# Performance work log

Hardware: AMD Instinct MI355X
Metric: run time of the kernel (lower is better)

## Reference

```python
import jax, jax.numpy as jnp
import numpy as np

R = 4            # num_runs
P_DROP = 0.2     # node dropout prob
BN_EPS = 1e-5
L = 2            # num_layers
D = 128          # hidden_channels
NA, NP_ = 50000, 100000
E = 500000


def setup_inputs() -> dict:
    key = jax.random.key(0)
    ks = jax.random.split(key, 20)
    s = 0.05
    x_author = jax.random.normal(ks[0], (NA, D), jnp.float32)
    x_paper = jax.random.normal(ks[1], (NP_, D), jnp.float32)
    # edge_index rows: [src, dst]
    ei_ap = jnp.stack([
        jax.random.randint(ks[2], (E,), 0, NA),
        jax.random.randint(ks[3], (E,), 0, NP_)]).astype(jnp.int64)
    ei_pa = jnp.stack([
        jax.random.randint(ks[4], (E,), 0, NP_),
        jax.random.randint(ks[5], (E,), 0, NA)]).astype(jnp.int64)
    # bernoulli(1-p) keep masks, one per run per node
    drop_author = (jax.random.uniform(ks[6], (R, NA)) < (1.0 - P_DROP)).astype(jnp.float32)
    drop_paper = (jax.random.uniform(ks[7], (R, NP_)) < (1.0 - P_DROP)).astype(jnp.float32)
    return {
        "x_author": x_author, "x_paper": x_paper,
        "ei_ap": ei_ap, "ei_pa": ei_pa,
        "drop_author": drop_author, "drop_paper": drop_paper,
        "lin_a_w": jax.random.normal(ks[8], (D, D)) * s,
        "lin_a_b": jnp.zeros((D,), jnp.float32),
        "lin_p_w": jax.random.normal(ks[9], (D, D)) * s,
        "lin_p_b": jnp.zeros((D,), jnp.float32),
        "W1": jax.random.normal(ks[10], (L, 2, D, D)) * s,
        "B1": jnp.zeros((L, 2, D), jnp.float32),
        "G": jnp.ones((L, 2, D), jnp.float32),
        "BT": jnp.zeros((L, 2, D), jnp.float32),
        "W2": jax.random.normal(ks[11], (L, 2, D, D)) * s,
        "B2": jnp.zeros((L, 2, D), jnp.float32),
        "EPS": jnp.zeros((L, 2), jnp.float32),  # GIN train_eps init 0
        "final_w": jax.random.normal(ks[12], (D, 4)) * s,
        "final_b": jnp.zeros((4,), jnp.float32),
    }


def _gin(x_src, x_dst, ei, eps, w1, b1, g, bt, w2, b2):
    # x_src: [Rs*Ns, D] flattened over runs; x_dst: [Rd*Nd, D]
    # scatter-sum neighbor messages into dst (only run-0 slots touched,
    # matching the original code which reuses the unexpanded edge_index)
    agg = jnp.zeros_like(x_dst).at[ei[1]].add(x_src[ei[0]])
    z = (1.0 + eps) * x_dst + agg
    h = z @ w1 + b1
    # BatchNorm1d, training-mode batch stats (biased variance)
    mu = h.mean(axis=0)
    var = ((h - mu) ** 2).mean(axis=0)
    h = (h - mu) * jax.lax.rsqrt(var + BN_EPS) * g + bt
    h = jax.nn.relu(h)
    return h @ w2 + b2


def reference(x_author, x_paper, ei_ap, ei_pa, drop_author, drop_paper,
              lin_a_w, lin_a_b, lin_p_w, lin_p_b,
              W1, B1, G, BT, W2, B2, EPS, final_w, final_b):
    inv_keep = 1.0 / (1.0 - P_DROP)
    # input projections, expand over runs, DropGNN node dropout
    h_a = x_author @ lin_a_w + lin_a_b                       # [Na, D]
    h_a = jnp.broadcast_to(h_a[None], (R,) + h_a.shape)      # [R, Na, D]
    h_a = h_a * drop_author[..., None] * inv_keep
    h_p = x_paper @ lin_p_w + lin_p_b
    h_p = jnp.broadcast_to(h_p[None], (R,) + h_p.shape)
    h_p = h_p * drop_paper[..., None] * inv_keep

    for l in range(L):
        xa = h_a.reshape(-1, D)
        xp = h_p.reshape(-1, D)
        # edge type 0: author -writes-> paper ; edge type 1: paper -> author
        new_p = _gin(xa, xp, ei_ap, EPS[l, 0], W1[l, 0], B1[l, 0], G[l, 0], BT[l, 0], W2[l, 0], B2[l, 0])
        new_a = _gin(xp, xa, ei_pa, EPS[l, 1], W1[l, 1], B1[l, 1], G[l, 1], BT[l, 1], W2[l, 1], B2[l, 1])
        h_a = jax.nn.relu(new_a.reshape(R, NA, D))
        h_p = jax.nn.relu(new_p.reshape(R, NP_, D))

    h = h_a.mean(axis=0)                                     # [Na, D]
    return h @ final_w + final_b                             # [Na, num_classes]
```

## Files before the change

### kernel.cpp

```cpp
#include <hip/hip_runtime.h>

#define NRUNS 4
#define NAU 50000
#define NPP 100000
#define NEDGE 500000
#define HD 128
#define INV_KEEP 1.25f
#define BN_EPS 1e-5f
#define LDA 136
#define NB_GEMM 1536

#define M_PROJ 0
#define M_GIN1 1
#define M_GIN2 2

typedef unsigned short bf16r;
typedef __attribute__((ext_vector_type(8))) short v8s;
typedef __attribute__((ext_vector_type(4))) float v4f;

__device__ inline float bf2f(bf16r u) {
    return __uint_as_float(((unsigned)u) << 16);
}
__device__ inline bf16r f2bf(float f) {
    __bf16 b = (__bf16)f;
    return __builtin_bit_cast(bf16r, b);
}

__global__ __launch_bounds__(256)
void zero_k(float* p, long n4) {
    long i = (long)blockIdx.x * 256 + threadIdx.x;
    long stride = (long)gridDim.x * 256;
    float4 z = make_float4(0.f, 0.f, 0.f, 0.f);
    for (; i < n4; i += stride) ((float4*)p)[i] = z;
}

__global__ __launch_bounds__(256)
void convw_k(const float* __restrict__ lin_a_w, const float* __restrict__ lin_p_w,
             const float* __restrict__ W1, const float* __restrict__ W2,
             bf16r* __restrict__ wt)
{
    int t = blockIdx.x >> 6;
    int e = (blockIdx.x & 63) * 256 + threadIdx.x;
    const float* src;
    if (t == 0) src = lin_a_w;
    else if (t == 1) src = lin_p_w;
    else if (t < 6) src = W1 + (size_t)(t - 2) * HD * HD;
    else src = W2 + (size_t)(t - 6) * HD * HD;
    int n = e >> 7, k = e & 127;
    wt[(size_t)t * HD * HD + e] = f2bf(src[(size_t)k * HD + n]);
}

__global__ __launch_bounds__(256)
void count_k(const int* __restrict__ ei, int E, int* cnt) {
    int e = blockIdx.x * 256 + threadIdx.x;
    if (e < E) atomicAdd(&cnt[ei[E + e]], 1);
}

__global__ __launch_bounds__(256)
void scan1_k(const int* __restrict__ in, int* out, int* partial, int n) {
    __shared__ int lds[256];
    int b = blockIdx.x, t = threadIdx.x;
    int base = b * 1024 + t * 4;
    int v0 = 0, v1 = 0, v2 = 0, v3 = 0;
    if (base + 3 < n) {
        int4 x = *(const int4*)(in + base);
        v0 = x.x; v1 = x.y; v2 = x.z; v3 = x.w;
    } else {
        if (base + 0 < n) v0 = in[base + 0];
        if (base + 1 < n) v1 = in[base + 1];
        if (base + 2 < n) v2 = in[base + 2];
        if (base + 3 < n) v3 = in[base + 3];
    }
    int s = v0 + v1 + v2 + v3;
    lds[t] = s;
    __syncthreads();
    for (int d = 1; d < 256; d <<= 1) {
        int x = (t >= d) ? lds[t - d] : 0;
        __syncthreads();
        lds[t] += x;
        __syncthreads();
    }
    int excl = lds[t] - s;
    if (base + 0 < n) out[base + 0] = excl;
    if (base + 1 < n) out[base + 1] = excl + v0;
    if (base + 2 < n) out[base + 2] = excl + v0 + v1;
    if (base + 3 < n) out[base + 3] = excl + v0 + v1 + v2;
    if (t == 255) partial[b] = lds[255];
}

__global__ __launch_bounds__(256)
void scan2_k(int* partial, int n) {
    __shared__ int lds[256];
    int t = threadIdx.x;
    int s = (t < n) ? partial[t] : 0;
    lds[t] = s;
    __syncthreads();
    for (int d = 1; d < 256; d <<= 1) {
        int x = (t >= d) ? lds[t - d] : 0;
        __syncthreads();
        lds[t] += x;
        __syncthreads();
    }
    if (t < n) partial[t] = lds[t] - s;
}

__global__ __launch_bounds__(256)
void scan3_k(int* off, int* cur, const int* __restrict__ partial, int n, int total) {
    int b = blockIdx.x, t = threadIdx.x;
    int add = partial[b];
    int base = b * 1024 + t * 4;
    #pragma unroll
    for (int j = 0; j < 4; ++j) {
        int i = base + j;
        if (i < n) {
            int v = off[i] + add;
            off[i] = v;
            cur[i] = v;
        }
    }
    if (b == 0 && t == 0) off[n] = total;
}

__global__ __launch_bounds__(256)
void fill_k(const int* __restrict__ ei, int E, int* cur, int* bucket) {
    int e = blockIdx.x * 256 + threadIdx.x;
    if (e < E) {
        int d = ei[E + e];
        int p = atomicAdd(&cur[d], 1);
        bucket[p] = ei[e];
    }
}

__global__ __launch_bounds__(256)
void gather2_k(const bf16r* __restrict__ hA, const bf16r* __restrict__ hP,
               bf16r* __restrict__ aggP, bf16r* __restrict__ aggA,
               const int* __restrict__ offAP, const int* __restrict__ bktAP,
               const int* __restrict__ offPA, const int* __restrict__ bktPA)
{
    int gw = (blockIdx.x * 256 + threadIdx.x) >> 6;
    int lane = threadIdx.x & 63;
    const bf16r* src; bf16r* agg; const int* off; const int* bkt; int w;
    if (gw < NPP) { src = hA; agg = aggP; off = offAP; bkt = bktAP; w = gw; }
    else          { src = hP; agg = aggA; off = offPA; bkt = bktPA; w = gw - NPP; }
    int s0 = off[w], s1 = off[w + 1];
    float a0 = 0.f, a1 = 0.f;
    int e = s0;
    for (; e + 1 < s1; e += 2) {
        int i0 = bkt[e], i1 = bkt[e + 1];
        ushort2 u = *(const ushort2*)(src + (size_t)i0 * HD + lane * 2);
        ushort2 v = *(const ushort2*)(src + (size_t)i1 * HD + lane * 2);
        a0 += bf2f(u.x) + bf2f(v.x);
        a1 += bf2f(u.y) + bf2f(v.y);
    }
    if (e < s1) {
        ushort2 u = *(const ushort2*)(src + (size_t)bkt[e] * HD + lane * 2);
        a0 += bf2f(u.x);
        a1 += bf2f(u.y);
    }
    ushort2 o;
    o.x = f2bf(a0);
    o.y = f2bf(a1);
    *(ushort2*)(agg + (size_t)w * HD + lane * 2) = o;
}

__global__ __launch_bounds__(256)
void scatter_k(const bf16r* __restrict__ src, float* dst,
               const int* __restrict__ ei, int E)
{
    int g = blockIdx.x * 256 + threadIdx.x;
    int e = g >> 5, lane = g & 31;
    if (e >= E) return;
    int s = ei[e], d = ei[E + e];
    ushort4 u = *(const ushort4*)(src + (size_t)s * HD + lane * 4);
    float* dp = dst + (size_t)d * HD + lane * 4;
    unsafeAtomicAdd(dp + 0, bf2f(u.x));
    unsafeAtomicAdd(dp + 1, bf2f(u.y));
    unsafeAtomicAdd(dp + 2, bf2f(u.z));
    unsafeAtomicAdd(dp + 3, bf2f(u.w));
}

struct SideP {
    const void* in;
    bf16r* out;
    const bf16r* wt;
    const float* bias;
    const void* agg;
    const float* epsp;
    float* gsum;
    float* gsumsq;
    const float* scale;
    const float* shift;
    const float* mask;
    int M, Nn, tiles;
};

template<int MODE, typename IT, typename AT>
__global__ __launch_bounds__(256)
void mfma_gemm(SideP P, SideP A, int BP)
{
    __shared__ bf16r za[64][LDA];
    __shared__ float red[2][HD];
    const int tid = threadIdx.x;

    SideP S;
    int t, tstride;
    if ((int)blockIdx.x < BP) { S = P; t = blockIdx.x; tstride = BP; }
    else { S = A; t = (int)blockIdx.x - BP; tstride = NB_GEMM - BP; }
    if (t >= S.tiles) return;

    const int wid = tid >> 6, lane = tid & 63;
    const int lr = lane & 15, lk = (lane >> 4) * 8;
    const int colq = (lane >> 4) * 4, cb = wid * 32;
    const int srow = tid >> 4;
    const int scol = (tid & 15) * 8;

    float epsv = 1.0f;
    if (MODE == M_GIN1) epsv = 1.0f + S.epsp[0];

    v8s w[2][4];
    #pragma unroll
    for (int cf = 0; cf < 2; ++cf)
        #pragma unroll
        for (int ks = 0; ks < 4; ++ks)
            w[cf][ks] = *(const v8s*)(S.wt + (size_t)(cb + cf * 16 + lr) * HD + ks * 32 + lk);

    const float4 bb0 = *(const float4*)(S.bias + cb + colq);
    const float4 bb1 = *(const float4*)(S.bias + cb + 16 + colq);

    float4 sc0h, sc1h, sh0h, sh1h;
    if (MODE == M_GIN2) {
        sc0h = *(const float4*)(S.scale + scol);
        sc1h = *(const float4*)(S.scale + scol + 4);
        sh0h = *(const float4*)(S.shift + scol);
        sh1h = *(const float4*)(S.shift + scol + 4);
    }

    float st_s[2][4], st_q[2][4];
    if (MODE == M_GIN1) {
        #pragma unroll
        for (int cf = 0; cf < 2; ++cf)
            #pragma unroll
            for (int j = 0; j < 4; ++j) { st_s[cf][j] = 0.f; st_q[cf][j] = 0.f; }
    }

    constexpr int NVH = (MODE == M_PROJ) ? 2 : 1;
    constexpr bool PAGG = (MODE == M_GIN1);
    constexpr int NVA = (PAGG && sizeof(AT) == 4) ? 2 : 1;
    int4 pre[4][NVH];
    int4 preA[4][NVA];

    auto prefetch = [&](int tt) {
        int m0n = tt * 64;
        #pragma unroll
        for (int i = 0; i < 4; ++i) {
            int gr = m0n + srow + 16 * i;
            if (gr < S.M) {
                const int4* p = (const int4*)((const IT*)S.in + (size_t)gr * HD + scol);
                pre[i][0] = p[0];
                if constexpr (NVH == 2) pre[i][1] = p[1];
            } else {
                pre[i][0] = make_int4(0, 0, 0, 0);
                if constexpr (NVH == 2) pre[i][1] = make_int4(0, 0, 0, 0);
            }
            if constexpr (PAGG) {
                if (gr < S.Nn) {
                    const int4* pa = (const int4*)((const AT*)S.agg + (size_t)gr * HD + scol);
                    preA[i][0] = pa[0];
                    if constexpr (NVA == 2) preA[i][1] = pa[1];
                } else {
                    preA[i][0] = make_int4(0, 0, 0, 0);
                    if constexpr (NVA == 2) preA[i][1] = make_int4(0, 0, 0, 0);
                }
            }
        }
    };

    prefetch(t);

    for (;;) {
        const int m0 = t * 64;
        #pragma unroll
        for (int i = 0; i < 4; ++i) {
            int row = srow + 16 * i;
            float v[8];
            if constexpr (NVH == 2) {
                const float* pf = (const float*)&pre[i][0];
                #pragma unroll
                for (int j = 0; j < 8; ++j) v[j] = pf[j];
            } else {
                const bf16r* pu = (const bf16r*)&pre[i][0];
                #pragma unroll
                for (int j = 0; j < 8; ++j) v[j] = bf2f(pu[j]);
            }
            if constexpr (MODE == M_GIN1) {
                float av[8];
                if constexpr (sizeof(AT) == 4) {
                    const float* pa = (const float*)&preA[i][0];
                    #pragma unroll
                    for (int j = 0; j < 8; ++j) av[j] = pa[j];
                } else {
                    const bf16r* pa = (const bf16r*)&preA[i][0];
                    #pragma unroll
                    for (int j = 0; j < 8; ++j) av[j] = bf2f(pa[j]);
                }
                #pragma unroll
                for (int j = 0; j < 8; ++j) v[j] = v[j] * epsv + av[j];
            } else if constexpr (MODE == M_GIN2) {
                v[0] = fmaxf(v[0] * sc0h.x + sh0h.x, 0.f);
                v[1] = fmaxf(v[1] * sc0h.y + sh0h.y, 0.f);
                v[2] = fmaxf(v[2] * sc0h.z + sh0h.z, 0.f);
                v[3] = fmaxf(v[3] * sc0h.w + sh0h.w, 0.f);
                v[4] = fmaxf(v[4] * sc1h.x + sh1h.x, 0.f);
                v[5] = fmaxf(v[5] * sc1h.y + sh1h.y, 0.f);
                v[6] = fmaxf(v[6] * sc1h.z + sh1h.z, 0.f);
                v[7] = fmaxf(v[7] * sc1h.w + sh1h.w, 0.f);
            }
            union { v8s w8; bf16r u[8]; } pk;
            #pragma unroll
            for (int j = 0; j < 8; ++j) pk.u[j] = f2bf(v[j]);
            *(v8s*)&za[row][scol] = pk.w8;
        }
        __syncthreads();

        const int tn = t + tstride;
        const bool more = tn < S.tiles;
        if (more) prefetch(tn);

        v4f acc[2][4];
        #pragma unroll
        for (int cf = 0; cf < 2; ++cf)
            #pragma unroll
            for (int rf = 0; rf < 4; ++rf) acc[cf][rf] = (v4f){0.f, 0.f, 0.f, 0.f};

        #pragma unroll
        for (int ks = 0; ks < 4; ++ks)
            #pragma unroll
            for (int rf = 0; rf < 4; ++rf) {
                v8s a = *(const v8s*)&za[rf * 16 + lr][ks * 32 + lk];
                acc[0][rf] = __builtin_amdgcn_mfma_f32_16x16x32_bf16(w[0][ks], a, acc[0][rf], 0, 0, 0);
                acc[1][rf] = __builtin_amdgcn_mfma_f32_16x16x32_bf16(w[1][ks], a, acc[1][rf], 0, 0, 0);
            }

        #pragma unroll
        for (int rf = 0; rf < 4; ++rf) {
            acc[0][rf][0] += bb0.x; acc[0][rf][1] += bb0.y;
            acc[0][rf][2] += bb0.z; acc[0][rf][3] += bb0.w;
            acc[1][rf][0] += bb1.x; acc[1][rf][1] += bb1.y;
            acc[1][rf][2] += bb1.z; acc[1][rf][3] += bb1.w;
        }

        if constexpr (MODE == M_PROJ) {
            #pragma unroll
            for (int rf = 0; rf < 4; ++rf) {
                int grow = m0 + rf * 16 + lr;
                if (grow < S.M) {
                    #pragma unroll
                    for (int run = 0; run < NRUNS; ++run) {
                        float wm = S.mask[(size_t)run * S.Nn + grow] * INV_KEEP;
                        #pragma unroll
                        for (int cf = 0; cf < 2; ++cf) {
                            ushort4 o;
                            o.x = f2bf(acc[cf][rf][0] * wm);
                            o.y = f2bf(acc[cf][rf][1] * wm);
                            o.z = f2bf(acc[cf][rf][2] * wm);
                            o.w = f2bf(acc[cf][rf][3] * wm);
                            *(ushort4*)(S.out + ((size_t)run * S.Nn + grow) * HD + cb + cf * 16 + colq) = o;
                        }
                    }
                }
            }
        } else if constexpr (MODE == M_GIN1) {
            #pragma unroll
            for (int rf = 0; rf < 4; ++rf) {
                int grow = m0 + rf * 16 + lr;
                #pragma unroll
                for (int cf = 0; cf < 2; ++cf) {
                    ushort4 o;
                    o.x = f2bf(acc[cf][rf][0]);
                    o.y = f2bf(acc[cf][rf][1]);
                    o.z = f2bf(acc[cf][rf][2]);
                    o.w = f2bf(acc[cf][rf][3]);
                    *(ushort4*)(S.out + (size_t)grow * HD + cb + cf * 16 + colq) = o;
                }
            }
            #pragma unroll
            for (int cf = 0; cf < 2; ++cf)
                #pragma unroll
                for (int j = 0; j < 4; ++j)
                    #pragma unroll
                    for (int rf = 0; rf < 4; ++rf) {
                        float vv = acc[cf][rf][j];
                        st_s[cf][j] += vv;
                        st_q[cf][j] += vv * vv;
                    }
        } else {
            #pragma unroll
            for (int rf = 0; rf < 4; ++rf) {
                int grow = m0 + rf * 16 + lr;
                #pragma unroll
                for (int cf = 0; cf < 2; ++cf) {
                    ushort4 o;
                    o.x = f2bf(fmaxf(acc[cf][rf][0], 0.f));
                    o.y = f2bf(fmaxf(acc[cf][rf][1], 0.f));
                    o.z = f2bf(fmaxf(acc[cf][rf][2], 0.f));
                    o.w = f2bf(fmaxf(acc[cf][rf][3], 0.f));
                    *(ushort4*)(S.out + (size_t)grow * HD + cb + cf * 16 + colq) = o;
                }
            }
        }

        if (!more) break;
        t = tn;
        __syncthreads();
    }

    if constexpr (MODE == M_GIN1) {
        #pragma unroll
        for (int d = 1; d < 16; d <<= 1)
            #pragma unroll
            for (int cf = 0; cf < 2; ++cf)
                #pragma unroll
                for (int j = 0; j < 4; ++j) {
                    st_s[cf][j] += __shfl_xor(st_s[cf][j], d);
                    st_q[cf][j] += __shfl_xor(st_q[cf][j], d);
                }
        if (lr == 0) {
            #pragma unroll
            for (int cf = 0; cf < 2; ++cf)
                #pragma unroll
                for (int j = 0; j < 4; ++j) {
                    red[0][cb + cf * 16 + colq + j] = st_s[cf][j];
                    red[1][cb + cf * 16 + colq + j] = st_q[cf][j];
                }
        }
        __syncthreads();
        if (tid < HD) {
            unsafeAtomicAdd(S.gsum + tid, red[0][tid]);
            unsafeAtomicAdd(S.gsumsq + tid, red[1][tid]);
        }
    }
}

__global__ void finalize2_k(float* gsP, float* gsqP, const float* gamP, const float* betP,
                            float* scP, float* shP, float invNP,
                            float* gsA, float* gsqA, const float* gamA, const float* betA,
                            float* scA, float* shA, float invNA)
{
    int c = threadIdx.x;
    float *gs, *gsq, *sc, *sh;
    const float *gm, *bt;
    float invN;
    if (c < HD) { gs = gsP; gsq = gsqP; gm = gamP; bt = betP; sc = scP; sh = shP; invN = invNP; }
    else { c -= HD; gs = gsA; gsq = gsqA; gm = gamA; bt = betA; sc = scA; sh = shA; invN = invNA; }
    float mu = gs[c] * invN;
    float var = gsq[c] * invN - mu * mu;
    float s = gm[c] * rsqrtf(var + BN_EPS);
    sc[c] = s;
    sh[c] = bt[c] - mu * s;
    gs[c] = 0.f;
    gsq[c] = 0.f;
}

__global__ __launch_bounds__(256)
void final_k(const bf16r* __restrict__ ha, const float* __restrict__ fw,
             const float* __restrict__ fb, float* __restrict__ out)
{
    int g = blockIdx.x * 256 + threadIdx.x;
    int node = g >> 6, lane = g & 63;
    if (node >= NAU) return;
    float m0 = 0.f, m1 = 0.f;
    #pragma unroll
    for (int r = 0; r < NRUNS; ++r) {
        size_t base = ((size_t)r * NAU + node) * HD;
        m0 += bf2f(ha[base + lane]);
        m1 += bf2f(ha[base + 64 + lane]);
    }
    m0 *= 0.25f;
    m1 *= 0.25f;
    float p[4];
    #pragma unroll
    for (int c = 0; c < 4; ++c)
        p[c] = m0 * fw[lane * 4 + c] + m1 * fw[(lane + 64) * 4 + c];
    #pragma unroll
    for (int off = 32; off >= 1; off >>= 1)
        #pragma unroll
        for (int c = 0; c < 4; ++c) p[c] += __shfl_down(p[c], off);
    if (lane == 0) {
        #pragma unroll
        for (int c = 0; c < 4; ++c) out[(size_t)node * 4 + c] = p[c] + fb[c];
    }
}

#define CSR_INTS ((size_t)(NPP + 4) + NEDGE + (NAU + 4) + NEDGE)
#define WT_ELEMS ((size_t)10 * HD * HD)

template<bool GATHER>
static void run_all(void* const* d_in, void* d_out, void* d_ws, hipStream_t stream)
{
    const float* x_author = (const float*)d_in[0];
    const float* x_paper  = (const float*)d_in[1];
    const int*   ei_ap    = (const int*)d_in[2];
    const int*   ei_pa    = (const int*)d_in[3];
    const float* drop_a   = (const float*)d_in[4];
    const float* drop_p   = (const float*)d_in[5];
    const float* lin_a_w  = (const float*)d_in[6];
    const float* lin_a_b  = (const float*)d_in[7];
    const float* lin_p_w  = (const float*)d_in[8];
    const float* lin_p_b  = (const float*)d_in[9];
    const float* W1       = (const float*)d_in[10];
    const float* B1       = (const float*)d_in[11];
    const float* G        = (const float*)d_in[12];
    const float* BT       = (const float*)d_in[13];
    const float* W2       = (const float*)d_in[14];
    const float* B2       = (const float*)d_in[15];
    const float* EPS      = (const float*)d_in[16];
    const float* fw       = (const float*)d_in[17];
    const float* fb       = (const float*)d_in[18];

    float* gsumP   = (float*)d_ws;
    float* gsumsqP = gsumP + HD;
    float* gsumA   = gsumP + 2 * HD;
    float* gsumsqA = gsumP + 3 * HD;
    float* scP     = gsumP + 4 * HD;
    float* shP     = gsumP + 5 * HD;
    float* scA     = gsumP + 6 * HD;
    float* shA     = gsumP + 7 * HD;
    bf16r* wt = (bf16r*)(gsumP + 8 * HD);
    char* cp = (char*)(wt + WT_ELEMS);

    int *off_ap = nullptr, *bkt_ap = nullptr, *off_pa = nullptr, *bkt_pa = nullptr;
    if (GATHER) {
        int* ip = (int*)cp;
        off_ap = ip;  ip += NPP + 4;
        bkt_ap = ip;  ip += NEDGE;
        off_pa = ip;  ip += NAU + 4;
        bkt_pa = ip;  ip += NEDGE;
        cp = (char*)ip;
    }
    void* agg_a_v = cp;
    size_t aggElem = GATHER ? sizeof(bf16r) : sizeof(float);
    void* agg_p_v = cp + (size_t)NAU * HD * aggElem;
    bf16r* h_a = (bf16r*)(cp + (size_t)(NAU + NPP) * HD * aggElem);
    bf16r* h_p = h_a + (size_t)NRUNS * NAU * HD;

    const bf16r* wt_lin_a = wt;
    const bf16r* wt_lin_p = wt + (size_t)1 * HD * HD;
    const bf16r* wt_W1    = wt + (size_t)2 * HD * HD;
    const bf16r* wt_W2    = wt + (size_t)6 * HD * HD;

    convw_k<<<640, 256, 0, stream>>>(lin_a_w, lin_p_w, W1, W2, wt);
    zero_k<<<1, 256, 0, stream>>>(gsumP, (4 * HD) / 4);

    if (GATHER) {
        int* cur_ap  = (int*)agg_a_v;
        int* cur_pa  = cur_ap + NPP;
        int* partial = cur_pa + NAU;
        {
            int nchunk = (NPP + 1023) / 1024;
            zero_k<<<64, 256, 0, stream>>>((float*)cur_ap, NPP / 4);
            count_k<<<(NEDGE + 255) / 256, 256, 0, stream>>>(ei_ap, NEDGE, cur_ap);
            scan1_k<<<nchunk, 256, 0, stream>>>(cur_ap, off_ap, partial, NPP);
            scan2_k<<<1, 256, 0, stream>>>(partial, nchunk);
            scan3_k<<<nchunk, 256, 0, stream>>>(off_ap, cur_ap, partial, NPP, NEDGE);
            fill_k<<<(NEDGE + 255) / 256, 256, 0, stream>>>(ei_ap, NEDGE, cur_ap, bkt_ap);
        }
        {
            int nchunk = (NAU + 1023) / 1024;
            zero_k<<<64, 256, 0, stream>>>((float*)cur_pa, NAU / 4);
            count_k<<<(NEDGE + 255) / 256, 256, 0, stream>>>(ei_pa, NEDGE, cur_pa);
            scan1_k<<<nchunk, 256, 0, stream>>>(cur_pa, off_pa, partial, NAU);
            scan2_k<<<1, 256, 0, stream>>>(partial, nchunk);
            scan3_k<<<nchunk, 256, 0, stream>>>(off_pa, cur_pa, partial, NAU, NEDGE);
            fill_k<<<(NEDGE + 255) / 256, 256, 0, stream>>>(ei_pa, NEDGE, cur_pa, bkt_pa);
        }
    }

    SideP Pp = {};
    Pp.in = x_paper; Pp.out = h_p; Pp.wt = wt_lin_p; Pp.bias = lin_p_b;
    Pp.mask = drop_p; Pp.M = NPP; Pp.Nn = NPP; Pp.tiles = (NPP + 63) / 64;
    SideP Pa = {};
    Pa.in = x_author; Pa.out = h_a; Pa.wt = wt_lin_a; Pa.bias = lin_a_b;
    Pa.mask = drop_a; Pa.M = NAU; Pa.Nn = NAU; Pa.tiles = (NAU + 63) / 64;
    int BPproj = (int)((long)NB_GEMM * Pp.tiles / (Pp.tiles + Pa.tiles));
    mfma_gemm<M_PROJ, float, bf16r><<<NB_GEMM, 256, 0, stream>>>(Pp, Pa, BPproj);

    const int TP = NRUNS * NPP / 64, TA = NRUNS * NAU / 64;
    const int BPgin = (int)((long)NB_GEMM * TP / (TP + TA));

    for (int l = 0; l < 2; ++l) {
        int t0 = l * 2 + 0, t1 = l * 2 + 1;

        if (GATHER) {
            gather2_k<<<((NPP + NAU) * 64) / 256, 256, 0, stream>>>(
                h_a, h_p, (bf16r*)agg_p_v, (bf16r*)agg_a_v,
                off_ap, bkt_ap, off_pa, bkt_pa);
        } else {
            zero_k<<<2048, 256, 0, stream>>>((float*)agg_a_v, ((size_t)(NAU + NPP) * HD) / 4);
            scatter_k<<<(NEDGE * 32) / 256, 256, 0, stream>>>(h_a, (float*)agg_p_v, ei_ap, NEDGE);
            scatter_k<<<(NEDGE * 32) / 256, 256, 0, stream>>>(h_p, (float*)agg_a_v, ei_pa, NEDGE);
        }

        SideP G1p = {};
        G1p.in = h_p; G1p.out = h_p; G1p.wt = wt_W1 + (size_t)t0 * HD * HD;
        G1p.bias = B1 + (size_t)t0 * HD; G1p.agg = agg_p_v; G1p.epsp = EPS + t0;
        G1p.gsum = gsumP; G1p.gsumsq = gsumsqP;
        G1p.M = NRUNS * NPP; G1p.Nn = NPP; G1p.tiles = TP;
        SideP G1a = {};
        G1a.in = h_a; G1a.out = h_a; G1a.wt = wt_W1 + (size_t)t1 * HD * HD;
        G1a.bias = B1 + (size_t)t1 * HD; G1a.agg = agg_a_v; G1a.epsp = EPS + t1;
        G1a.gsum = gsumA; G1a.gsumsq = gsumsqA;
        G1a.M = NRUNS * NAU; G1a.Nn = NAU; G1a.tiles = TA;
        if (GATHER)
            mfma_gemm<M_GIN1, bf16r, bf16r><<<NB_GEMM, 256, 0, stream>>>(G1p, G1a, BPgin);
        else
            mfma_gemm<M_GIN1, bf16r, float><<<NB_GEMM, 256, 0, stream>>>(G1p, G1a, BPgin);

        finalize2_k<<<1, 256, 0, stream>>>(
            gsumP, gsumsqP, G + (size_t)t0 * HD, BT + (size_t)t0 * HD, scP, shP,
            1.0f / (NRUNS * NPP),
            gsumA, gsumsqA, G + (size_t)t1 * HD, BT + (size_t)t1 * HD, scA, shA,
            1.0f / (NRUNS * NAU));

        SideP G2p = {};
        G2p.in = h_p; G2p.out = h_p; G2p.wt = wt_W2 + (size_t)t0 * HD * HD;
        G2p.bias = B2 + (size_t)t0 * HD; G2p.scale = scP; G2p.shift = shP;
        G2p.M = NRUNS * NPP; G2p.Nn = NPP; G2p.tiles = TP;
        SideP G2a = {};
        G2a.in = h_a; G2a.out = h_a; G2a.wt = wt_W2 + (size_t)t1 * HD * HD;
        G2a.bias = B2 + (size_t)t1 * HD; G2a.scale = scA; G2a.shift = shA;
        G2a.M = NRUNS * NAU; G2a.Nn = NAU; G2a.tiles = TA;
        mfma_gemm<M_GIN2, bf16r, bf16r><<<NB_GEMM, 256, 0, stream>>>(G2p, G2a, BPgin);
    }

    final_k<<<(NAU * 64) / 256, 256, 0, stream>>>(h_a, fw, fb, (float*)d_out);
}

extern "C" void kernel_launch(void* const* d_in, const int* in_sizes, int n_in,
                              void* d_out, int out_size, void* d_ws, size_t ws_size,
                              hipStream_t stream)
{
    const size_t hB    = (size_t)NRUNS * (NAU + NPP) * HD * sizeof(bf16r);
    const size_t statB = 8 * HD * sizeof(float);
    const size_t wtB   = WT_ELEMS * sizeof(bf16r);
    const size_t csrB  = CSR_INTS * sizeof(int);
    const size_t aggBF = (size_t)(NAU + NPP) * HD * sizeof(bf16r);

    const size_t need_gather = statB + wtB + csrB + aggBF + hB;
    if (ws_size >= need_gather) {
        run_all<true>(d_in, d_out, d_ws, stream);
    } else {
        run_all<false>(d_in, d_out, d_ws, stream);
    }
}
```

Measured before the change: 650.0 us.

## Store unexpanded projections and apply dropout masks lazily in gather and GIN1

The input projection now writes a single unexpanded bf16 copy per node type instead of materialising four masked run copies. The dropout mask and keep scaling are applied on the fly, inside the layer-0 gather (per source node) and inside the first GIN GEMM prologue (per run row). This cuts the write traffic of the projection stage and the read footprint of the first gather. It also lowers NB_GEMM from 1536 to 1280 and keeps the old path only for the non-gather fallback, which now uses a float agg type in M_PROJ.

```diff
diff --git a/kernel.cpp b/kernel.cpp
--- a/kernel.cpp
+++ b/kernel.cpp
@@ -8,11 +8,13 @@
 #define INV_KEEP 1.25f
 #define BN_EPS 1e-5f
 #define LDA 136
-#define NB_GEMM 1536
-
-#define M_PROJ 0
-#define M_GIN1 1
-#define M_GIN2 2
+#define NB_GEMM 1280
+
+#define M_PROJ  0
+#define M_GIN1  1
+#define M_GIN2  2
+#define M_PROJ1 3
+#define M_GIN1M 4
 
 typedef unsigned short bf16r;
 typedef __attribute__((ext_vector_type(8))) short v8s;
@@ -131,17 +133,20 @@
     }
 }
 
+template<bool MASKED>
 __global__ __launch_bounds__(256)
 void gather2_k(const bf16r* __restrict__ hA, const bf16r* __restrict__ hP,
                bf16r* __restrict__ aggP, bf16r* __restrict__ aggA,
                const int* __restrict__ offAP, const int* __restrict__ bktAP,
-               const int* __restrict__ offPA, const int* __restrict__ bktPA)
+               const int* __restrict__ offPA, const int* __restrict__ bktPA,
+               const float* __restrict__ mA0, const float* __restrict__ mP0)
 {
     int gw = (blockIdx.x * 256 + threadIdx.x) >> 6;
     int lane = threadIdx.x & 63;
-    const bf16r* src; bf16r* agg; const int* off; const int* bkt; int w;
-    if (gw < NPP) { src = hA; agg = aggP; off = offAP; bkt = bktAP; w = gw; }
-    else          { src = hP; agg = aggA; off = offPA; bkt = bktPA; w = gw - NPP; }
+    const bf16r* src; bf16r* agg; const int* off; const int* bkt;
+    const float* msk; int w;
+    if (gw < NPP) { src = hA; agg = aggP; off = offAP; bkt = bktAP; msk = mA0; w = gw; }
+    else          { src = hP; agg = aggA; off = offPA; bkt = bktPA; msk = mP0; w = gw - NPP; }
     int s0 = off[w], s1 = off[w + 1];
     float a0 = 0.f, a1 = 0.f;
     int e = s0;
@@ -149,13 +154,21 @@
         int i0 = bkt[e], i1 = bkt[e + 1];
         ushort2 u = *(const ushort2*)(src + (size_t)i0 * HD + lane * 2);
         ushort2 v = *(const ushort2*)(src + (size_t)i1 * HD + lane * 2);
-        a0 += bf2f(u.x) + bf2f(v.x);
-        a1 += bf2f(u.y) + bf2f(v.y);
+        if constexpr (MASKED) {
+            float m0 = msk[i0] * INV_KEEP, m1 = msk[i1] * INV_KEEP;
+            a0 += m0 * bf2f(u.x) + m1 * bf2f(v.x);
+            a1 += m0 * bf2f(u.y) + m1 * bf2f(v.y);
+        } else {
+            a0 += bf2f(u.x) + bf2f(v.x);
+            a1 += bf2f(u.y) + bf2f(v.y);
+        }
     }
     if (e < s1) {
-        ushort2 u = *(const ushort2*)(src + (size_t)bkt[e] * HD + lane * 2);
-        a0 += bf2f(u.x);
-        a1 += bf2f(u.y);
+        int i0 = bkt[e];
+        ushort2 u = *(const ushort2*)(src + (size_t)i0 * HD + lane * 2);
+        float m0 = MASKED ? msk[i0] * INV_KEEP : 1.0f;
+        a0 += m0 * bf2f(u.x);
+        a1 += m0 * bf2f(u.y);
     }
     ushort2 o;
     o.x = f2bf(a0);
@@ -214,8 +227,10 @@
     const int srow = tid >> 4;
     const int scol = (tid & 15) * 8;
 
+    constexpr bool GIN1ANY = (MODE == M_GIN1 || MODE == M_GIN1M);
+
     float epsv = 1.0f;
-    if (MODE == M_GIN1) epsv = 1.0f + S.epsp[0];
+    if (GIN1ANY) epsv = 1.0f + S.epsp[0];
 
     v8s w[2][4];
     #pragma unroll
@@ -236,25 +251,33 @@
     }
 
     float st_s[2][4], st_q[2][4];
-    if (MODE == M_GIN1) {
+    if (GIN1ANY) {
         #pragma unroll
         for (int cf = 0; cf < 2; ++cf)
             #pragma unroll
             for (int j = 0; j < 4; ++j) { st_s[cf][j] = 0.f; st_q[cf][j] = 0.f; }
     }
 
-    constexpr int NVH = (MODE == M_PROJ) ? 2 : 1;
-    constexpr bool PAGG = (MODE == M_GIN1);
+    constexpr int NVH = (MODE == M_PROJ || MODE == M_PROJ1) ? 2 : 1;
+    constexpr bool PAGG = GIN1ANY;
+    constexpr bool PMSK = (MODE == M_GIN1M);
     constexpr int NVA = (PAGG && sizeof(AT) == 4) ? 2 : 1;
     int4 pre[4][NVH];
     int4 preA[4][NVA];
+    float mpre[PMSK ? 4 : 1];
 
     auto prefetch = [&](int tt) {
         int m0n = tt * 64;
         #pragma unroll
         for (int i = 0; i < 4; ++i) {
             int gr = m0n + srow + 16 * i;
-            if (gr < S.M) {
+            if constexpr (PMSK) {
+                int run = (gr >= S.Nn) + (gr >= 2 * S.Nn) + (gr >= 3 * S.Nn);
+                int node = gr - run * S.Nn;
+                mpre[i] = S.mask[gr];
+                const int4* p = (const int4*)((const IT*)S.in + (size_t)node * HD + scol);
+                pre[i][0] = p[0];
+            } else if (gr < S.M) {
                 const int4* p = (const int4*)((const IT*)S.in + (size_t)gr * HD + scol);
                 pre[i][0] = p[0];
                 if constexpr (NVH == 2) pre[i][1] = p[1];
@@ -292,7 +315,7 @@
                 #pragma unroll
                 for (int j = 0; j < 8; ++j) v[j] = bf2f(pu[j]);
             }
-            if constexpr (MODE == M_GIN1) {
+            if constexpr (MODE == M_GIN1 || MODE == M_GIN1M) {
                 float av[8];
                 if constexpr (sizeof(AT) == 4) {
                     const float* pa = (const float*)&preA[i][0];
@@ -303,8 +326,10 @@
                     #pragma unroll
                     for (int j = 0; j < 8; ++j) av[j] = bf2f(pa[j]);
                 }
+                float coef = epsv;
+                if constexpr (PMSK) coef = mpre[i] * (INV_KEEP)*epsv;
                 #pragma unroll
-                for (int j = 0; j < 8; ++j) v[j] = v[j] * epsv + av[j];
+                for (int j = 0; j < 8; ++j) v[j] = v[j] * coef + av[j];
             } else if constexpr (MODE == M_GIN2) {
                 v[0] = fmaxf(v[0] * sc0h.x + sh0h.x, 0.f);
                 v[1] = fmaxf(v[1] * sc0h.y + sh0h.y, 0.f);
@@ -369,7 +394,23 @@
                     }
                 }
             }
-        } else if constexpr (MODE == M_GIN1) {
+        } else if constexpr (MODE == M_PROJ1) {
+            #pragma unroll
+            for (int rf = 0; rf < 4; ++rf) {
+                int grow = m0 + rf * 16 + lr;
+                if (grow < S.M) {
+                    #pragma unroll
+                    for (int cf = 0; cf < 2; ++cf) {
+                        ushort4 o;
+                        o.x = f2bf(acc[cf][rf][0]);
+                        o.y = f2bf(acc[cf][rf][1]);
+                        o.z = f2bf(acc[cf][rf][2]);
+                        o.w = f2bf(acc[cf][rf][3]);
+                        *(ushort4*)(S.out + (size_t)grow * HD + cb + cf * 16 + colq) = o;
+                    }
+                }
+            }
+        } else if constexpr (GIN1ANY) {
             #pragma unroll
             for (int rf = 0; rf < 4; ++rf) {
                 int grow = m0 + rf * 16 + lr;
@@ -414,7 +455,7 @@
         __syncthreads();
     }
 
-    if constexpr (MODE == M_GIN1) {
+    if constexpr (GIN1ANY) {
         #pragma unroll
         for (int d = 1; d < 16; d <<= 1)
             #pragma unroll
@@ -540,7 +581,13 @@
     void* agg_a_v = cp;
     size_t aggElem = GATHER ? sizeof(bf16r) : sizeof(float);
     void* agg_p_v = cp + (size_t)NAU * HD * aggElem;
-    bf16r* h_a = (bf16r*)(cp + (size_t)(NAU + NPP) * HD * aggElem);
+    cp += (size_t)(NAU + NPP) * HD * aggElem;
+    bf16r* proj_a = nullptr; bf16r* proj_p = nullptr;
+    if (GATHER) {
+        proj_a = (bf16r*)cp;  cp += (size_t)NAU * HD * sizeof(bf16r);
+        proj_p = (bf16r*)cp;  cp += (size_t)NPP * HD * sizeof(bf16r);
+    }
+    bf16r* h_a = (bf16r*)cp;
     bf16r* h_p = h_a + (size_t)NRUNS * NAU * HD;
 
     const bf16r* wt_lin_a = wt;
@@ -575,61 +622,108 @@
         }
     }
 
-    SideP Pp = {};
-    Pp.in = x_paper; Pp.out = h_p; Pp.wt = wt_lin_p; Pp.bias = lin_p_b;
-    Pp.mask = drop_p; Pp.M = NPP; Pp.Nn = NPP; Pp.tiles = (NPP + 63) / 64;
-    SideP Pa = {};
-    Pa.in = x_author; Pa.out = h_a; Pa.wt = wt_lin_a; Pa.bias = lin_a_b;
-    Pa.mask = drop_a; Pa.M = NAU; Pa.Nn = NAU; Pa.tiles = (NAU + 63) / 64;
-    int BPproj = (int)((long)NB_GEMM * Pp.tiles / (Pp.tiles + Pa.tiles));
-    mfma_gemm<M_PROJ, float, bf16r><<<NB_GEMM, 256, 0, stream>>>(Pp, Pa, BPproj);
-
     const int TP = NRUNS * NPP / 64, TA = NRUNS * NAU / 64;
     const int BPgin = (int)((long)NB_GEMM * TP / (TP + TA));
 
-    for (int l = 0; l < 2; ++l) {
-        int t0 = l * 2 + 0, t1 = l * 2 + 1;
-
-        if (GATHER) {
-            gather2_k<<<((NPP + NAU) * 64) / 256, 256, 0, stream>>>(
-                h_a, h_p, (bf16r*)agg_p_v, (bf16r*)agg_a_v,
-                off_ap, bkt_ap, off_pa, bkt_pa);
-        } else {
+    if (GATHER) {
+        SideP Pp = {};
+        Pp.in = x_paper; Pp.out = proj_p; Pp.wt = wt_lin_p; Pp.bias = lin_p_b;
+        Pp.M = NPP; Pp.Nn = NPP; Pp.tiles = (NPP + 63) / 64;
+        SideP Pa = {};
+        Pa.in = x_author; Pa.out = proj_a; Pa.wt = wt_lin_a; Pa.bias = lin_a_b;
+        Pa.M = NAU; Pa.Nn = NAU; Pa.tiles = (NAU + 63) / 64;
+        int BPproj = (int)((long)NB_GEMM * Pp.tiles / (Pp.tiles + Pa.tiles));
+        mfma_gemm<M_PROJ1, float, bf16r><<<NB_GEMM, 256, 0, stream>>>(Pp, Pa, BPproj);
+
+        for (int l = 0; l < 2; ++l) {
+            int t0 = l * 2 + 0, t1 = l * 2 + 1;
+
+            if (l == 0) {
+                gather2_k<true><<<((NPP + NAU) * 64) / 256, 256, 0, stream>>>(
+                    proj_a, proj_p, (bf16r*)agg_p_v, (bf16r*)agg_a_v,
+                    off_ap, bkt_ap, off_pa, bkt_pa, drop_a, drop_p);
+            } else {
+                gather2_k<false><<<((NPP + NAU) * 64) / 256, 256, 0, stream>>>(
+                    h_a, h_p, (bf16r*)agg_p_v, (bf16r*)agg_a_v,
+                    off_ap, bkt_ap, off_pa, bkt_pa, nullptr, nullptr);
+            }
+
+            SideP G1p = {}, G1a = {};
+            G1p.wt = wt_W1 + (size_t)t0 * HD * HD;
+            G1p.bias = B1 + (size_t)t0 * HD; G1p.agg = agg_p_v; G1p.epsp = EPS + t0;
+            G1p.gsum = gsumP; G1p.gsumsq = gsumsqP;
+            G1p.M = NRUNS * NPP; G1p.Nn = NPP; G1p.tiles = TP; G1p.out = h_p;
+            G1a.wt = wt_W1 + (size_t)t1 * HD * HD;
+            G1a.bias = B1 + (size_t)t1 * HD; G1a.agg = agg_a_v; G1a.epsp = EPS + t1;
+            G1a.gsum = gsumA; G1a.gsumsq = gsumsqA;
+            G1a.M = NRUNS * NAU; G1a.Nn = NAU; G1a.tiles = TA; G1a.out = h_a;
+            if (l == 0) {
+                G1p.in = proj_p; G1p.mask = drop_p;
+                G1a.in = proj_a; G1a.mask = drop_a;
+                mfma_gemm<M_GIN1M, bf16r, bf16r><<<NB_GEMM, 256, 0, stream>>>(G1p, G1a, BPgin);
+            } else {
+                G1p.in = h_p;
+                G1a.in = h_a;
+                mfma_gemm<M_GIN1, bf16r, bf16r><<<NB_GEMM, 256, 0, stream>>>(G1p, G1a, BPgin);
+            }
+
+            finalize2_k<<<1, 256, 0, stream>>>(
+                gsumP, gsumsqP, G + (size_t)t0 * HD, BT + (size_t)t0 * HD, scP, shP,
+                1.0f / (NRUNS * NPP),
+                gsumA, gsumsqA, G + (size_t)t1 * HD, BT + (size_t)t1 * HD, scA, shA,
+                1.0f / (NRUNS * NAU));
+
+            SideP G2p = {}, G2a = {};
+            G2p.in = h_p; G2p.out = h_p; G2p.wt = wt_W2 + (size_t)t0 * HD * HD;
+            G2p.bias = B2 + (size_t)t0 * HD; G2p.scale = scP; G2p.shift = shP;
+            G2p.M = NRUNS * NPP; G2p.Nn = NPP; G2p.tiles = TP;
+            G2a.in = h_a; G2a.out = h_a; G2a.wt = wt_W2 + (size_t)t1 * HD * HD;
+            G2a.bias = B2 + (size_t)t1 * HD; G2a.scale = scA; G2a.shift = shA;
+            G2a.M = NRUNS * NAU; G2a.Nn = NAU; G2a.tiles = TA;
+            mfma_gemm<M_GIN2, bf16r, bf16r><<<NB_GEMM, 256, 0, stream>>>(G2p, G2a, BPgin);
+        }
+    } else {
+        SideP Pp = {};
+        Pp.in = x_paper; Pp.out = h_p; Pp.wt = wt_lin_p; Pp.bias = lin_p_b;
+        Pp.mask = drop_p; Pp.M = NPP; Pp.Nn = NPP; Pp.tiles = (NPP + 63) / 64;
+        SideP Pa = {};
+        Pa.in = x_author; Pa.out = h_a; Pa.wt = wt_lin_a; Pa.bias = lin_a_b;
+        Pa.mask = drop_a; Pa.M = NAU; Pa.Nn = NAU; Pa.tiles = (NAU + 63) / 64;
+        int BPproj = (int)((long)NB_GEMM * Pp.tiles / (Pp.tiles + Pa.tiles));
+        mfma_gemm<M_PROJ, float, float><<<NB_GEMM, 256, 0, stream>>>(Pp, Pa, BPproj);
+
+        for (int l = 0; l < 2; ++l) {
+            int t0 = l * 2 + 0, t1 = l * 2 + 1;
             zero_k<<<2048, 256, 0, stream>>>((float*)agg_a_v, ((size_t)(NAU + NPP) * HD) / 4);
             scatter_k<<<(NEDGE * 32) / 256, 256, 0, stream>>>(h_a, (float*)agg_p_v, ei_ap, NEDGE);
             scatter_k<<<(NEDGE * 32) / 256, 256, 0, stream>>>(h_p, (float*)agg_a_v, ei_pa, NEDGE);
-        }
-
-        SideP G1p = {};
-        G1p.in = h_p; G1p.out = h_p; G1p.wt = wt_W1 + (size_t)t0 * HD * HD;
-        G1p.bias = B1 + (size_t)t0 * HD; G1p.agg = agg_p_v; G1p.epsp = EPS + t0;
-        G1p.gsum = gsumP; G1p.gsumsq = gsumsqP;
-        G1p.M = NRUNS * NPP; G1p.Nn = NPP; G1p.tiles = TP;
-        SideP G1a = {};
-        G1a.in = h_a; G1a.out = h_a; G1a.wt = wt_W1 + (size_t)t1 * HD * HD;
-        G1a.bias = B1 + (size_t)t1 * HD; G1a.agg = agg_a_v; G1a.epsp = EPS + t1;
-        G1a.gsum = gsumA; G1a.gsumsq = gsumsqA;
-        G1a.M = NRUNS * NAU; G1a.Nn = NAU; G1a.tiles = TA;
-        if (GATHER)
-            mfma_gemm<M_GIN1, bf16r, bf16r><<<NB_GEMM, 256, 0, stream>>>(G1p, G1a, BPgin);
-        else
+
+            SideP G1p = {}, G1a = {};
+            G1p.in = h_p; G1p.out = h_p; G1p.wt = wt_W1 + (size_t)t0 * HD * HD;
+            G1p.bias = B1 + (size_t)t0 * HD; G1p.agg = agg_p_v; G1p.epsp = EPS + t0;
+            G1p.gsum = gsumP; G1p.gsumsq = gsumsqP;
+            G1p.M = NRUNS * NPP; G1p.Nn = NPP; G1p.tiles = TP;
+            G1a.in = h_a; G1a.out = h_a; G1a.wt = wt_W1 + (size_t)t1 * HD * HD;
+            G1a.bias = B1 + (size_t)t1 * HD; G1a.agg = agg_a_v; G1a.epsp = EPS + t1;
+            G1a.gsum = gsumA; G1a.gsumsq = gsumsqA;
+            G1a.M = NRUNS * NAU; G1a.Nn = NAU; G1a.tiles = TA;
             mfma_gemm<M_GIN1, bf16r, float><<<NB_GEMM, 256, 0, stream>>>(G1p, G1a, BPgin);
 
-        finalize2_k<<<1, 256, 0, stream>>>(
-            gsumP, gsumsqP, G + (size_t)t0 * HD, BT + (size_t)t0 * HD, scP, shP,
-            1.0f / (NRUNS * NPP),
-            gsumA, gsumsqA, G + (size_t)t1 * HD, BT + (size_t)t1 * HD, scA, shA,
-            1.0f / (NRUNS * NAU));
-
-        SideP G2p = {};
-        G2p.in = h_p; G2p.out = h_p; G2p.wt = wt_W2 + (size_t)t0 * HD * HD;
-        G2p.bias = B2 + (size_t)t0 * HD; G2p.scale = scP; G2p.shift = shP;
-        G2p.M = NRUNS * NPP; G2p.Nn = NPP; G2p.tiles = TP;
-        SideP G2a = {};
-        G2a.in = h_a; G2a.out = h_a; G2a.wt = wt_W2 + (size_t)t1 * HD * HD;
-        G2a.bias = B2 + (size_t)t1 * HD; G2a.scale = scA; G2a.shift = shA;
-        G2a.M = NRUNS * NAU; G2a.Nn = NAU; G2a.tiles = TA;
-        mfma_gemm<M_GIN2, bf16r, bf16r><<<NB_GEMM, 256, 0, stream>>>(G2p, G2a, BPgin);
+            finalize2_k<<<1, 256, 0, stream>>>(
+                gsumP, gsumsqP, G + (size_t)t0 * HD, BT + (size_t)t0 * HD, scP, shP,
+                1.0f / (NRUNS * NPP),
+                gsumA, gsumsqA, G + (size_t)t1 * HD, BT + (size_t)t1 * HD, scA, shA,
+                1.0f / (NRUNS * NAU));
+
+            SideP G2p = {}, G2a = {};
+            G2p.in = h_p; G2p.out = h_p; G2p.wt = wt_W2 + (size_t)t0 * HD * HD;
+            G2p.bias = B2 + (size_t)t0 * HD; G2p.scale = scP; G2p.shift = shP;
+            G2p.M = NRUNS * NPP; G2p.Nn = NPP; G2p.tiles = TP;
+            G2a.in = h_a; G2a.out = h_a; G2a.wt = wt_W2 + (size_t)t1 * HD * HD;
+            G2a.bias = B2 + (size_t)t1 * HD; G2a.scale = scA; G2a.shift = shA;
+            G2a.M = NRUNS * NAU; G2a.Nn = NAU; G2a.tiles = TA;
+            mfma_gemm<M_GIN2, bf16r, bf16r><<<NB_GEMM, 256, 0, stream>>>(G2p, G2a, BPgin);
+        }
     }
 
     final_k<<<(NAU * 64) / 256, 256, 0, stream>>>(h_a, fw, fb, (float*)d_out);
@@ -644,8 +738,9 @@
     const size_t wtB   = WT_ELEMS * sizeof(bf16r);
     const size_t csrB  = CSR_INTS * sizeof(int);
     const size_t aggBF = (size_t)(NAU + NPP) * HD * sizeof(bf16r);
-
-    const size_t need_gather = statB + wtB + csrB + aggBF + hB;
+    const size_t projB = (size_t)(NAU + NPP) * HD * sizeof(bf16r);
+
+    const size_t need_gather = statB + wtB + csrB + aggBF + projB + hB;
     if (ws_size >= need_gather) {
         run_all<true>(d_in, d_out, d_ws, stream);
     } else {
```

Result: faster. 626.9 us (-3.6%).
